# Kernel optimization log

Hardware: AMD Instinct MI355X
Metric: run time of the kernel (lower is better)

## Reference

```python
import jax, jax.numpy as jnp
import numpy as np

N = 100000    # total nodes
E = 1600000   # total edges
B = 64        # graphs in batch
F_IN = 64     # node feature dim (input_shape)
F_E = 16      # edge feature dim (edge_shape)
A = 6         # action dim (action_shape)
H = 16        # hidden_channels
L = 4         # num GEN layers
EPS = 1e-7    # GENConv message eps


def _ln(x, g, b):
    mu = x.mean(-1, keepdims=True)
    var = x.var(-1, keepdims=True)
    return (x - mu) * jax.lax.rsqrt(var + 1e-5) * g + b


def _genconv(x, src, dst, ea, t, w1, b1, g1, be1, w2, b2):
    # GENConv with softmax aggregation: msg = relu(x_j + e) + eps,
    # alpha = scatter_softmax(t*msg, dst), aggr = scatter_sum(msg*alpha),
    # out = MLP(x + aggr) with MLP = Lin(H,2H) -> LN -> ReLU -> Lin(2H,H)
    msg = jax.nn.relu(x[src] + ea) + EPS                      # [E,H]
    z = t * msg
    m = jax.ops.segment_max(z, dst, num_segments=N)           # [N,H]
    e = jnp.exp(z - m[dst])
    s = jax.ops.segment_sum(e, dst, num_segments=N)
    alpha = e / (s[dst] + 1e-16)
    aggr = jax.ops.segment_sum(msg * alpha, dst, num_segments=N)
    h = x + aggr
    h = jax.nn.relu(_ln(h @ w1 + b1, g1, be1))
    return h @ w2 + b2


def setup_inputs() -> dict:
    key = jax.random.key(0)
    ks = jax.random.split(key, 20)
    def rn(k, shape, scale=0.1):
        return jax.random.normal(k, shape, dtype=jnp.float32) * scale
    return {
        "x": rn(ks[0], (N, F_IN), 1.0),
        "edge_attr": rn(ks[1], (E, F_E), 1.0),
        "edge_index": jax.random.randint(ks[2], (2, E), 0, N),
        "batch": (jnp.arange(N) * B) // N,  # sorted, every graph non-empty
        "action": rn(ks[3], (B, A), 1.0),
        "node_w": rn(ks[4], (F_IN, H)), "node_b": rn(ks[5], (H,)),
        "edge_w": rn(ks[6], (F_E, H)), "edge_b": rn(ks[7], (H,)),
        "t": jnp.ones((L,), jnp.float32),
        "mlp_w1": rn(ks[8], (L, H, 2 * H)), "mlp_b1": rn(ks[9], (L, 2 * H)),
        "mlp_g1": jnp.ones((L, 2 * H), jnp.float32),
        "mlp_be1": jnp.zeros((L, 2 * H), jnp.float32),
        "mlp_w2": rn(ks[10], (L, 2 * H, H)), "mlp_b2": rn(ks[11], (L, H)),
        "ln_g": jnp.ones((L, H), jnp.float32), "ln_b": jnp.zeros((L, H), jnp.float32),
        "pin_w": rn(ks[12], (2 * H, 128)), "pin_b": rn(ks[13], (128,)),
        "ph_w": rn(ks[14], (128 + A, 10)), "ph_b": rn(ks[15], (10,)),
        "po_w": rn(ks[16], (10, 1)), "po_b": rn(ks[17], (1,)),
    }


def reference(x, edge_attr, edge_index, batch, action, node_w, node_b, edge_w,
              edge_b, t, mlp_w1, mlp_b1, mlp_g1, mlp_be1, mlp_w2, mlp_b2,
              ln_g, ln_b, pin_w, pin_b, ph_w, ph_b, po_w, po_b):
    src, dst = edge_index[0], edge_index[1]
    h = x @ node_w + node_b
    ea = edge_attr @ edge_w + edge_b
    # layer 0: bare conv (as in original forward)
    h = _genconv(h, src, dst, ea, t[0], mlp_w1[0], mlp_b1[0], mlp_g1[0],
                 mlp_be1[0], mlp_w2[0], mlp_b2[0])
    # layers 1..3: DeepGCN 'res+' blocks: x + conv(relu(norm(x)))
    for i in range(1, L):
        y = jax.nn.relu(_ln(h, ln_g[i], ln_b[i]))
        h = h + _genconv(y, src, dst, ea, t[i], mlp_w1[i], mlp_b1[i],
                         mlp_g1[i], mlp_be1[i], mlp_w2[i], mlp_b2[i])
    # final norm + act from layer 0 (dropout disabled: eval mode)
    h = jax.nn.relu(_ln(h, ln_g[0], ln_b[0]))
    # global max + mean pooling per graph
    gmp = jax.ops.segment_max(h, batch, num_segments=B)
    cnt = jax.ops.segment_sum(jnp.ones((N, 1), h.dtype), batch, num_segments=B)
    gap = jax.ops.segment_sum(h, batch, num_segments=B) / cnt
    mol = jnp.concatenate([gmp, gap], axis=1)                 # [B, 32]
    fp = jax.nn.relu(mol @ pin_w + pin_b)                     # [B, 128]
    pol = jax.nn.relu(jnp.concatenate([fp, action], axis=1) @ ph_w + ph_b)
    return pol @ po_w + po_b                                  # [B, 1]
```

## Files before the change

### kernel.cpp

```cpp
#include <hip/hip_runtime.h>
#include <hip/hip_fp16.h>

#define N_NODES 100000
#define N_EDGES 1600000
#define NB 64
#define F_INn 64
#define HID 16
#define NL 4
#define NSCAN_BLK 391
#define NBIN 256
#define BINW 391
#define NPBLK 256

__device__ __forceinline__ unsigned pack2h(float a, float b) {
    __half2 h = __floats2half2_rn(a, b);
    return *reinterpret_cast<unsigned*>(&h);
}

__device__ __forceinline__ void blk_range(int blk, int& e0, int& e1) {
    e0 = (int)(((long long)blk * N_EDGES) / NPBLK);
    e1 = (int)(((long long)(blk + 1) * N_EDGES) / NPBLK);
}

__global__ __launch_bounds__(256) void k_embed(
    const float* __restrict__ x, const float* __restrict__ nw,
    const float* __restrict__ nb, float* __restrict__ yout)
{
    __shared__ float xs[16 * 64];
    __shared__ float Wn[64 * 16];
    __shared__ float Bn[16];
    const int tid = threadIdx.x;
    for (int i = tid; i < 1024; i += 256) Wn[i] = nw[i];
    if (tid < 16) Bn[tid] = nb[tid];
    const int n0 = blockIdx.x * 16;
    reinterpret_cast<float4*>(xs)[tid] =
        reinterpret_cast<const float4*>(x + (size_t)n0 * F_INn)[tid];
    __syncthreads();
    const int nl = tid >> 4, j = tid & 15;
    float acc = Bn[j];
    #pragma unroll 8
    for (int k = 0; k < 64; ++k) acc += xs[nl * 64 + k] * Wn[k * 16 + j];
    yout[(size_t)(n0 + nl) * HID + j] = acc;
}

__global__ __launch_bounds__(256) void k_hist1(
    const int* __restrict__ dstA, int* __restrict__ histG)
{
    __shared__ int h[NBIN];
    const int tid = threadIdx.x, blk = blockIdx.x;
    for (int t = tid; t < NBIN; t += 256) h[t] = 0;
    __syncthreads();
    int e0, e1; blk_range(blk, e0, e1);
    for (int e = e0 + tid; e < e1; e += 256)
        atomicAdd(&h[dstA[e] / BINW], 1);
    __syncthreads();
    for (int t = tid; t < NBIN; t += 256) histG[blk * NBIN + t] = h[t];
}

__global__ __launch_bounds__(NPBLK) void k_scanblk(
    const int* __restrict__ histG, int* __restrict__ boffsG,
    int* __restrict__ binTot)
{
    __shared__ int sc[NPBLK];
    const int tid = threadIdx.x, bin = blockIdx.x;
    const int v = histG[tid * NBIN + bin];
    sc[tid] = v;
    __syncthreads();
    for (int off = 1; off < NPBLK; off <<= 1) {
        int t = (tid >= off) ? sc[tid - off] : 0;
        __syncthreads();
        sc[tid] += t;
        __syncthreads();
    }
    boffsG[tid * NBIN + bin] = sc[tid] - v;
    if (tid == NPBLK - 1) binTot[bin] = sc[tid];
}

__global__ __launch_bounds__(NBIN) void k_scanbin(
    const int* __restrict__ binTot, int* __restrict__ binStart)
{
    __shared__ int sc[NBIN];
    const int tid = threadIdx.x;
    const int v = binTot[tid];
    sc[tid] = v;
    __syncthreads();
    for (int off = 1; off < NBIN; off <<= 1) {
        int t = (tid >= off) ? sc[tid - off] : 0;
        __syncthreads();
        sc[tid] += t;
        __syncthreads();
    }
    binStart[tid] = sc[tid] - v;
    if (tid == NBIN - 1) binStart[NBIN] = sc[tid];
}

__global__ __launch_bounds__(256) void k_partl(
    const int* __restrict__ dstA, const int* __restrict__ srcA,
    const int* __restrict__ boffsG, const int* __restrict__ binStart,
    int2* __restrict__ partK)
{
    __shared__ int cur[NBIN];
    const int tid = threadIdx.x, blk = blockIdx.x;
    for (int t = tid; t < NBIN; t += 256)
        cur[t] = binStart[t] + boffsG[blk * NBIN + t];
    __syncthreads();
    int e0, e1; blk_range(blk, e0, e1);
    for (int e = e0 + tid; e < e1; e += 256) {
        const int d = dstA[e];
        const int bin = d / BINW;
        const int dloc = d - bin * BINW;
        const int p = atomicAdd(&cur[bin], 1);
        partK[p] = make_int2(srcA[e], (dloc << 21) | e);
    }
}

__global__ __launch_bounds__(512) void k_finishl(
    const int2* __restrict__ partK, const int* __restrict__ binStart,
    int* __restrict__ rowptr, int* __restrict__ srcP, int* __restrict__ csrE)
{
    __shared__ int h[BINW];
    __shared__ int sc[512];
    __shared__ int cur[BINW];
    const int tid = threadIdx.x, bin = blockIdx.x;
    const int base = bin * BINW;
    for (int t = tid; t < BINW; t += 512) h[t] = 0;
    __syncthreads();
    const int i0 = binStart[bin], i1 = binStart[bin + 1];
    for (int i = i0 + tid; i < i1; i += 512)
        atomicAdd(&h[partK[i].y >> 21], 1);
    __syncthreads();
    const int v = (tid < BINW) ? h[tid] : 0;
    sc[tid] = v;
    __syncthreads();
    for (int off = 1; off < 512; off <<= 1) {
        int t = (tid >= off) ? sc[tid - off] : 0;
        __syncthreads();
        sc[tid] += t;
        __syncthreads();
    }
    if (tid < BINW) {
        const int r = i0 + sc[tid] - v;
        const int idx = base + tid;
        if (idx < N_NODES) rowptr[idx] = r;
        cur[tid] = r;
    }
    if (bin == NBIN - 1 && tid == 0) rowptr[N_NODES] = N_EDGES;
    __syncthreads();
    for (int i = i0 + tid; i < i1; i += 512) {
        const int2 w = partK[i];
        const int dloc = w.y >> 21;
        const int p = atomicAdd(&cur[dloc], 1);
        srcP[p] = w.x;
        csrE[p] = w.y & 0x1FFFFF;
    }
}

__global__ __launch_bounds__(256) void k_permea(
    const int* __restrict__ csrE, const float* __restrict__ eattr,
    const float* __restrict__ ew, const float* __restrict__ ebv,
    __half* __restrict__ eaPh)
{
    __shared__ float EW[256];
    __shared__ float EB[16];
    const int tid = threadIdx.x;
    EW[tid] = ew[tid];
    if (tid < 16) EB[tid] = ebv[tid];
    __syncthreads();
    const int p = blockIdx.x * 256 + tid;
    const int e = csrE[p];
    float acc[16];
    #pragma unroll
    for (int j = 0; j < 16; ++j) acc[j] = EB[j];
    const float4* ag = reinterpret_cast<const float4*>(eattr + ((size_t)e << 4));
    #pragma unroll
    for (int q = 0; q < 4; ++q) {
        const float4 av = ag[q];
        #pragma unroll
        for (int j = 0; j < 16; ++j) {
            acc[j] += av.x * EW[(q * 4 + 0) * 16 + j];
            acc[j] += av.y * EW[(q * 4 + 1) * 16 + j];
            acc[j] += av.z * EW[(q * 4 + 2) * 16 + j];
            acc[j] += av.w * EW[(q * 4 + 3) * 16 + j];
        }
    }
    uint4 lo, hi;
    lo.x = pack2h(acc[0], acc[1]);   lo.y = pack2h(acc[2], acc[3]);
    lo.z = pack2h(acc[4], acc[5]);   lo.w = pack2h(acc[6], acc[7]);
    hi.x = pack2h(acc[8], acc[9]);   hi.y = pack2h(acc[10], acc[11]);
    hi.z = pack2h(acc[12], acc[13]); hi.w = pack2h(acc[14], acc[15]);
    uint4* eo = reinterpret_cast<uint4*>(eaPh) + ((size_t)p << 1);
    eo[0] = lo;
    eo[1] = hi;
}

__global__ __launch_bounds__(256) void k_count(
    const int* __restrict__ dstA, int* __restrict__ cnt)
{
    const int e = blockIdx.x * 256 + threadIdx.x;
    if (e < N_EDGES) atomicAdd(cnt + dstA[e], 1);
}

__global__ __launch_bounds__(256) void k_scan1(
    const int* __restrict__ cnt, int* __restrict__ rowptr, int* __restrict__ bsum)
{
    __shared__ int sc[256];
    const int tid = threadIdx.x;
    const int i = blockIdx.x * 256 + tid;
    const int v = (i < N_NODES) ? cnt[i] : 0;
    sc[tid] = v;
    __syncthreads();
    for (int off = 1; off < 256; off <<= 1) {
        int t = (tid >= off) ? sc[tid - off] : 0;
        __syncthreads();
        sc[tid] += t;
        __syncthreads();
    }
    if (i < N_NODES) rowptr[i] = sc[tid] - v;
    if (tid == 255) bsum[blockIdx.x] = sc[tid];
}

__global__ __launch_bounds__(512) void k_scan2(
    const int* __restrict__ bsum, int* __restrict__ offs, int* __restrict__ rowptr)
{
    __shared__ int sc[512];
    const int tid = threadIdx.x;
    const int v = (tid < NSCAN_BLK) ? bsum[tid] : 0;
    sc[tid] = v;
    __syncthreads();
    for (int off = 1; off < 512; off <<= 1) {
        int t = (tid >= off) ? sc[tid - off] : 0;
        __syncthreads();
        sc[tid] += t;
        __syncthreads();
    }
    if (tid < NSCAN_BLK) offs[tid] = sc[tid] - v;
    if (tid == NSCAN_BLK - 1) rowptr[N_NODES] = sc[tid];
}

__global__ __launch_bounds__(256) void k_scan3(
    int* __restrict__ rowptr, const int* __restrict__ offs, int* __restrict__ cnt)
{
    const int i = blockIdx.x * 256 + threadIdx.x;
    if (i < N_NODES) {
        rowptr[i] += offs[i >> 8];
        cnt[i] = 0;
    }
}

__global__ __launch_bounds__(256) void k_fill(
    const int* __restrict__ dstA, const int* __restrict__ rowptr,
    int* __restrict__ cnt, int* __restrict__ csr)
{
    const int e = blockIdx.x * 256 + threadIdx.x;
    if (e >= N_EDGES) return;
    const int d = dstA[e];
    const int pos = atomicAdd(cnt + d, 1);
    csr[rowptr[d] + pos] = e;
}

__global__ __launch_bounds__(256, 8) void k_aggr(
    const float* __restrict__ yin, const int* __restrict__ rowptr,
    const int* __restrict__ srcP, const __half* __restrict__ eaPh,
    const float* __restrict__ tArr, int layer, float* __restrict__ aggr)
{
    const int t = blockIdx.x * 256 + threadIdx.x;
    const int n = t >> 4;
    if (n >= N_NODES) return;
    const int sub = threadIdx.x & 15;
    const int es = sub >> 2, cg = sub & 3;
    const int row0 = rowptr[n], row1 = rowptr[n + 1];
    const float tv = tArr[layer];

    float4 s = make_float4(0.f, 0.f, 0.f, 0.f);
    float4 num = make_float4(0.f, 0.f, 0.f, 0.f);

    int i = row0 + es;
    bool has = (i < row1);
    int spn = 0;
    uint2 ean = make_uint2(0u, 0u);
    if (has) {
        spn = srcP[i];
        ean = reinterpret_cast<const uint2*>(eaPh + ((size_t)i << 4))[cg];
    }
    while (has) {
        const int sp = spn;
        const uint2 eaw = ean;
        const int i2 = i + 4;
        const bool has2 = (i2 < row1);
        if (has2) {
            spn = srcP[i2];
            ean = reinterpret_cast<const uint2*>(eaPh + ((size_t)i2 << 4))[cg];
        }
        const float4 yv = reinterpret_cast<const float4*>(yin + ((size_t)sp << 4))[cg];
        const float2 f0 = __half22float2(*reinterpret_cast<const __half2*>(&eaw.x));
        const float2 f1 = __half22float2(*reinterpret_cast<const __half2*>(&eaw.y));
        float m, ez;
        m = fmaxf(yv.x + f0.x, 0.f) + 1e-7f; ez = __expf(tv * m); s.x += ez; num.x += m * ez;
        m = fmaxf(yv.y + f0.y, 0.f) + 1e-7f; ez = __expf(tv * m); s.y += ez; num.y += m * ez;
        m = fmaxf(yv.z + f1.x, 0.f) + 1e-7f; ez = __expf(tv * m); s.z += ez; num.z += m * ez;
        m = fmaxf(yv.w + f1.y, 0.f) + 1e-7f; ez = __expf(tv * m); s.w += ez; num.w += m * ez;
        i = i2; has = has2;
    }
    s.x += __shfl_xor(s.x, 4); s.y += __shfl_xor(s.y, 4);
    s.z += __shfl_xor(s.z, 4); s.w += __shfl_xor(s.w, 4);
    num.x += __shfl_xor(num.x, 4); num.y += __shfl_xor(num.y, 4);
    num.z += __shfl_xor(num.z, 4); num.w += __shfl_xor(num.w, 4);
    s.x += __shfl_xor(s.x, 8); s.y += __shfl_xor(s.y, 8);
    s.z += __shfl_xor(s.z, 8); s.w += __shfl_xor(s.w, 8);
    num.x += __shfl_xor(num.x, 8); num.y += __shfl_xor(num.y, 8);
    num.z += __shfl_xor(num.z, 8); num.w += __shfl_xor(num.w, 8);
    if (es == 0) {
        float4 r;
        r.x = num.x / (s.x + 1e-16f);
        r.y = num.y / (s.y + 1e-16f);
        r.z = num.z / (s.z + 1e-16f);
        r.w = num.w / (s.w + 1e-16f);
        reinterpret_cast<float4*>(aggr + ((size_t)n << 4))[cg] = r;
    }
}

__global__ __launch_bounds__(256) void k_node(
    const float* __restrict__ yin, const float* __restrict__ hprev,
    const float* __restrict__ aggr,
    const float* __restrict__ w1, const float* __restrict__ b1,
    const float* __restrict__ g1, const float* __restrict__ be1,
    const float* __restrict__ w2, const float* __restrict__ b2,
    const float* __restrict__ gn, const float* __restrict__ bn,
    float* __restrict__ hout, float* __restrict__ yout, int layer)
{
    __shared__ float4 W1[128];
    __shared__ float4 W2[128];
    __shared__ float B1[32], G1[32], BE1[32], B2[16], GN[16], BN[16];
    const int tid = threadIdx.x;
    if (tid < 128) {
        W1[tid] = reinterpret_cast<const float4*>(w1)[tid];
        W2[tid] = reinterpret_cast<const float4*>(w2)[tid];
    }
    if (tid < 32) { B1[tid] = b1[tid]; G1[tid] = g1[tid]; BE1[tid] = be1[tid]; }
    if (tid < 16) { B2[tid] = b2[tid]; GN[tid] = gn[tid]; BN[tid] = bn[tid]; }
    __syncthreads();
    const int n = blockIdx.x * 256 + tid;
    if (n >= N_NODES) return;
    const size_t base = (size_t)n * HID;

    float hin[16];
    {
        const float4* yg = reinterpret_cast<const float4*>(yin + base);
        const float4* ag = reinterpret_cast<const float4*>(aggr + base);
        #pragma unroll
        for (int q = 0; q < 4; ++q) {
            float4 yv = yg[q], av = ag[q];
            hin[q * 4 + 0] = yv.x + av.x;
            hin[q * 4 + 1] = yv.y + av.y;
            hin[q * 4 + 2] = yv.z + av.z;
            hin[q * 4 + 3] = yv.w + av.w;
        }
    }
    float z[32];
    #pragma unroll
    for (int i = 0; i < 32; ++i) z[i] = B1[i];
    #pragma unroll
    for (int j = 0; j < 16; ++j) {
        const float hv = hin[j];
        #pragma unroll
        for (int q = 0; q < 8; ++q) {
            float4 w = W1[j * 8 + q];
            z[q * 4 + 0] += hv * w.x; z[q * 4 + 1] += hv * w.y;
            z[q * 4 + 2] += hv * w.z; z[q * 4 + 3] += hv * w.w;
        }
    }
    float mu = 0.f;
    #pragma unroll
    for (int i = 0; i < 32; ++i) mu += z[i];
    mu *= (1.f / 32.f);
    float var = 0.f;
    #pragma unroll
    for (int i = 0; i < 32; ++i) { float d = z[i] - mu; var += d * d; }
    var *= (1.f / 32.f);
    const float rs = rsqrtf(var + 1e-5f);

    float o[16];
    #pragma unroll
    for (int j = 0; j < 16; ++j) o[j] = B2[j];
    #pragma unroll
    for (int i = 0; i < 32; ++i) {
        const float r = fmaxf((z[i] - mu) * rs * G1[i] + BE1[i], 0.f);
        #pragma unroll
        for (int q = 0; q < 4; ++q) {
            float4 w = W2[i * 4 + q];
            o[q * 4 + 0] += r * w.x; o[q * 4 + 1] += r * w.y;
            o[q * 4 + 2] += r * w.z; o[q * 4 + 3] += r * w.w;
        }
    }
    float hn[16];
    if (layer == 0) {
        #pragma unroll
        for (int j = 0; j < 16; ++j) hn[j] = o[j];
    } else {
        const float4* hg = reinterpret_cast<const float4*>(hprev + base);
        float hr[16];
        *reinterpret_cast<float4*>(&hr[0])  = hg[0];
        *reinterpret_cast<float4*>(&hr[4])  = hg[1];
        *reinterpret_cast<float4*>(&hr[8])  = hg[2];
        *reinterpret_cast<float4*>(&hr[12]) = hg[3];
        #pragma unroll
        for (int j = 0; j < 16; ++j) hn[j] = hr[j] + o[j];
    }
    {
        float4* ho = reinterpret_cast<float4*>(hout + base);
        #pragma unroll
        for (int q = 0; q < 4; ++q)
            ho[q] = make_float4(hn[q*4+0], hn[q*4+1], hn[q*4+2], hn[q*4+3]);
    }
    float mu2 = 0.f;
    #pragma unroll
    for (int j = 0; j < 16; ++j) mu2 += hn[j];
    mu2 *= (1.f / 16.f);
    float v2 = 0.f;
    #pragma unroll
    for (int j = 0; j < 16; ++j) { float d = hn[j] - mu2; v2 += d * d; }
    v2 *= (1.f / 16.f);
    const float rs2 = rsqrtf(v2 + 1e-5f);
    float yn[16];
    #pragma unroll
    for (int j = 0; j < 16; ++j)
        yn[j] = fmaxf((hn[j] - mu2) * rs2 * GN[j] + BN[j], 0.f);
    {
        float4* yo = reinterpret_cast<float4*>(yout + base);
        #pragma unroll
        for (int q = 0; q < 4; ++q)
            yo[q] = make_float4(yn[q*4+0], yn[q*4+1], yn[q*4+2], yn[q*4+3]);
    }
}

__global__ __launch_bounds__(256) void k_layer(
    const float* __restrict__ yin, const float* __restrict__ hprev,
    const int* __restrict__ rowptr, const int* __restrict__ csr,
    const int* __restrict__ srcA, const float* __restrict__ eattr,
    const float* __restrict__ ew, const float* __restrict__ ebv,
    const float* __restrict__ tArr, int layer,
    const float* __restrict__ w1, const float* __restrict__ b1,
    const float* __restrict__ g1, const float* __restrict__ be1,
    const float* __restrict__ w2, const float* __restrict__ b2,
    const float* __restrict__ gn, const float* __restrict__ bn,
    float* __restrict__ hout, float* __restrict__ yout)
{
    __shared__ float EW[256];
    __shared__ float EB[16];
    __shared__ float4 W1[128];
    __shared__ float4 W2[128];
    __shared__ float B1[32], G1[32], BE1[32], B2[16], GN[16], BN[16];
    const int tid = threadIdx.x;
    EW[tid] = ew[tid];
    if (tid < 128) {
        W1[tid] = reinterpret_cast<const float4*>(w1)[tid];
        W2[tid] = reinterpret_cast<const float4*>(w2)[tid];
    }
    if (tid < 32) { B1[tid] = b1[tid]; G1[tid] = g1[tid]; BE1[tid] = be1[tid]; }
    if (tid < 16) { EB[tid] = ebv[tid]; B2[tid] = b2[tid]; GN[tid] = gn[tid]; BN[tid] = bn[tid]; }
    __syncthreads();

    const int t = blockIdx.x * 256 + tid;
    const int n = t >> 2, sub = t & 3;
    if (n >= N_NODES) return;
    const int row0 = rowptr[n], row1 = rowptr[n + 1];
    const float tv = tArr[layer];

    float s[16], num[16];
    #pragma unroll
    for (int j = 0; j < 16; ++j) { s[j] = 0.f; num[j] = 0.f; }

    for (int i = row0 + sub; i < row1; i += 4) {
        const int eid = csr[i];
        const int sp = srcA[eid];
        float a[16], yv[16];
        {
            const float4* ag = reinterpret_cast<const float4*>(eattr + (size_t)eid * 16);
            *reinterpret_cast<float4*>(&a[0])  = ag[0];
            *reinterpret_cast<float4*>(&a[4])  = ag[1];
            *reinterpret_cast<float4*>(&a[8])  = ag[2];
            *reinterpret_cast<float4*>(&a[12]) = ag[3];
            const float4* yg = reinterpret_cast<const float4*>(yin + (size_t)sp * 16);
            *reinterpret_cast<float4*>(&yv[0])  = yg[0];
            *reinterpret_cast<float4*>(&yv[4])  = yg[1];
            *reinterpret_cast<float4*>(&yv[8])  = yg[2];
            *reinterpret_cast<float4*>(&yv[12]) = yg[3];
        }
        float acc[16];
        #pragma unroll
        for (int j = 0; j < 16; ++j) acc[j] = EB[j];
        #pragma unroll
        for (int k = 0; k < 16; ++k) {
            const float av = a[k];
            #pragma unroll
            for (int j = 0; j < 16; ++j) acc[j] += av * EW[k * 16 + j];
        }
        #pragma unroll
        for (int j = 0; j < 16; ++j) {
            float m = fmaxf(yv[j] + acc[j], 0.f) + 1e-7f;
            float ez = __expf(tv * m);
            s[j] += ez;
            num[j] += m * ez;
        }
    }
    #pragma unroll
    for (int j = 0; j < 16; ++j) {
        s[j]   += __shfl_xor(s[j], 1);   num[j] += __shfl_xor(num[j], 1);
        s[j]   += __shfl_xor(s[j], 2);   num[j] += __shfl_xor(num[j], 2);
    }
    if (sub != 0) return;

    const size_t base = (size_t)n * HID;
    float hin[16];
    {
        const float4* yg = reinterpret_cast<const float4*>(yin + base);
        float yr[16];
        *reinterpret_cast<float4*>(&yr[0])  = yg[0];
        *reinterpret_cast<float4*>(&yr[4])  = yg[1];
        *reinterpret_cast<float4*>(&yr[8])  = yg[2];
        *reinterpret_cast<float4*>(&yr[12]) = yg[3];
        #pragma unroll
        for (int j = 0; j < 16; ++j) hin[j] = yr[j] + num[j] / (s[j] + 1e-16f);
    }
    float z[32];
    #pragma unroll
    for (int i = 0; i < 32; ++i) z[i] = B1[i];
    #pragma unroll
    for (int j = 0; j < 16; ++j) {
        const float hv = hin[j];
        #pragma unroll
        for (int q = 0; q < 8; ++q) {
            float4 w = W1[j * 8 + q];
            z[q * 4 + 0] += hv * w.x; z[q * 4 + 1] += hv * w.y;
            z[q * 4 + 2] += hv * w.z; z[q * 4 + 3] += hv * w.w;
        }
    }
    float mu = 0.f;
    #pragma unroll
    for (int i = 0; i < 32; ++i) mu += z[i];
    mu *= (1.f / 32.f);
    float var = 0.f;
    #pragma unroll
    for (int i = 0; i < 32; ++i) { float d = z[i] - mu; var += d * d; }
    var *= (1.f / 32.f);
    const float rs = rsqrtf(var + 1e-5f);

    float o[16];
    #pragma unroll
    for (int j = 0; j < 16; ++j) o[j] = B2[j];
    #pragma unroll
    for (int i = 0; i < 32; ++i) {
        const float r = fmaxf((z[i] - mu) * rs * G1[i] + BE1[i], 0.f);
        #pragma unroll
        for (int q = 0; q < 4; ++q) {
            float4 w = W2[i * 4 + q];
            o[q * 4 + 0] += r * w.x; o[q * 4 + 1] += r * w.y;
            o[q * 4 + 2] += r * w.z; o[q * 4 + 3] += r * w.w;
        }
    }
    float hn[16];
    if (layer == 0) {
        #pragma unroll
        for (int j = 0; j < 16; ++j) hn[j] = o[j];
    } else {
        const float4* hg = reinterpret_cast<const float4*>(hprev + base);
        float hr[16];
        *reinterpret_cast<float4*>(&hr[0])  = hg[0];
        *reinterpret_cast<float4*>(&hr[4])  = hg[1];
        *reinterpret_cast<float4*>(&hr[8])  = hg[2];
        *reinterpret_cast<float4*>(&hr[12]) = hg[3];
        #pragma unroll
        for (int j = 0; j < 16; ++j) hn[j] = hr[j] + o[j];
    }
    {
        float4* ho = reinterpret_cast<float4*>(hout + base);
        #pragma unroll
        for (int q = 0; q < 4; ++q)
            ho[q] = make_float4(hn[q*4+0], hn[q*4+1], hn[q*4+2], hn[q*4+3]);
    }
    float mu2 = 0.f;
    #pragma unroll
    for (int j = 0; j < 16; ++j) mu2 += hn[j];
    mu2 *= (1.f / 16.f);
    float v2 = 0.f;
    #pragma unroll
    for (int j = 0; j < 16; ++j) { float d = hn[j] - mu2; v2 += d * d; }
    v2 *= (1.f / 16.f);
    const float rs2 = rsqrtf(v2 + 1e-5f);
    float yn[16];
    #pragma unroll
    for (int j = 0; j < 16; ++j)
        yn[j] = fmaxf((hn[j] - mu2) * rs2 * GN[j] + BN[j], 0.f);
    {
        float4* yo = reinterpret_cast<float4*>(yout + base);
        #pragma unroll
        for (int q = 0; q < 4; ++q)
            yo[q] = make_float4(yn[q*4+0], yn[q*4+1], yn[q*4+2], yn[q*4+3]);
    }
}

__global__ __launch_bounds__(256) void k_pool(
    const float* __restrict__ y, const int* __restrict__ batch,
    float* __restrict__ gmax, float* __restrict__ gsum, float* __restrict__ gcnt)
{
    const int g = blockIdx.x;
    const int tid = threadIdx.x;
    int lo = 0, hi = N_NODES;
    while (lo < hi) { int mid = (lo + hi) >> 1; if (batch[mid] < g) lo = mid + 1; else hi = mid; }
    const int start = lo;
    lo = 0; hi = N_NODES;
    while (lo < hi) { int mid = (lo + hi) >> 1; if (batch[mid] < g + 1) lo = mid + 1; else hi = mid; }
    const int end = lo;

    const int ch = tid & 15, slot = tid >> 4;
    float mx = 0.f, sm = 0.f;
    for (int n = start + slot; n < end; n += 16) {
        float v = y[(size_t)n * HID + ch];
        mx = fmaxf(mx, v);
        sm += v;
    }
    __shared__ float rm[256], rsum[256];
    rm[tid] = mx; rsum[tid] = sm;
    __syncthreads();
    for (int off = 8; off >= 1; off >>= 1) {
        if (slot < off) {
            rm[tid] = fmaxf(rm[tid], rm[tid + off * 16]);
            rsum[tid] += rsum[tid + off * 16];
        }
        __syncthreads();
    }
    if (slot == 0) {
        gmax[g * HID + ch] = rm[ch];
        gsum[g * HID + ch] = rsum[ch];
        if (ch == 0) gcnt[g] = (float)(end - start);
    }
}

__global__ __launch_bounds__(128) void k_final(
    const float* __restrict__ gmax, const float* __restrict__ gsum,
    const float* __restrict__ gcnt, const float* __restrict__ action,
    const float* __restrict__ pin_w, const float* __restrict__ pin_b,
    const float* __restrict__ ph_w, const float* __restrict__ ph_b,
    const float* __restrict__ po_w, const float* __restrict__ po_b,
    float* __restrict__ out)
{
    __shared__ float mol[32];
    __shared__ float fpv[128];
    __shared__ float pol[10];
    const int b = blockIdx.x, tid = threadIdx.x;
    if (tid < 16) mol[tid] = gmax[b * 16 + tid];
    else if (tid < 32) mol[tid] = gsum[b * 16 + (tid - 16)] / gcnt[b];
    __syncthreads();
    float acc = pin_b[tid];
    #pragma unroll 4
    for (int k = 0; k < 32; ++k) acc += mol[k] * pin_w[k * 128 + tid];
    fpv[tid] = fmaxf(acc, 0.f);
    __syncthreads();
    if (tid < 10) {
        float a2 = ph_b[tid];
        for (int k = 0; k < 128; ++k) a2 += fpv[k] * ph_w[k * 10 + tid];
        #pragma unroll
        for (int k = 0; k < 6; ++k) a2 += action[b * 6 + k] * ph_w[(128 + k) * 10 + tid];
        pol[tid] = fmaxf(a2, 0.f);
    }
    __syncthreads();
    if (tid == 0) {
        float o = po_b[0];
        #pragma unroll
        for (int i = 0; i < 10; ++i) o += pol[i] * po_w[i];
        out[b] = o;
    }
}

extern "C" void kernel_launch(void* const* d_in, const int* in_sizes, int n_in,
                              void* d_out, int out_size, void* d_ws, size_t ws_size,
                              hipStream_t stream)
{
    const float* x       = (const float*)d_in[0];
    const float* eattr   = (const float*)d_in[1];
    const int*   eidx    = (const int*)d_in[2];
    const int*   batch   = (const int*)d_in[3];
    const float* action  = (const float*)d_in[4];
    const float* node_w  = (const float*)d_in[5];
    const float* node_b  = (const float*)d_in[6];
    const float* edge_w  = (const float*)d_in[7];
    const float* edge_b  = (const float*)d_in[8];
    const float* tArr    = (const float*)d_in[9];
    const float* mlp_w1  = (const float*)d_in[10];
    const float* mlp_b1  = (const float*)d_in[11];
    const float* mlp_g1  = (const float*)d_in[12];
    const float* mlp_be1 = (const float*)d_in[13];
    const float* mlp_w2  = (const float*)d_in[14];
    const float* mlp_b2  = (const float*)d_in[15];
    const float* ln_g    = (const float*)d_in[16];
    const float* ln_b    = (const float*)d_in[17];
    const float* pin_w   = (const float*)d_in[18];
    const float* pin_b   = (const float*)d_in[19];
    const float* ph_w    = (const float*)d_in[20];
    const float* ph_b    = (const float*)d_in[21];
    const float* po_w    = (const float*)d_in[22];
    const float* po_b    = (const float*)d_in[23];
    float* out = (float*)d_out;

    char* ws = (char*)d_ws;
    float* h      = (float*)ws;
    float* y      = h + (size_t)N_NODES * HID;
    float* aggr   = y + (size_t)N_NODES * HID;
    int*   cnt    = (int*)(aggr + (size_t)N_NODES * HID);
    int*   rowptr = cnt + N_NODES;
    int*   bsum   = rowptr + N_NODES + 1;
    int*   offs   = bsum + NSCAN_BLK;
    int*   csr    = offs + NSCAN_BLK + 1;
    float* gmax   = (float*)(csr + N_EDGES);
    float* gsum   = gmax + NB * HID;
    float* gcnt   = gsum + NB * HID;
    int*   srcP   = (int*)(gcnt + NB);
    int*   csrE   = srcP + N_EDGES;
    __half* eaPh  = (__half*)(csrE + N_EDGES);
    const size_t need = (size_t)((char*)(eaPh + (size_t)N_EDGES * HID) - ws);
    const bool fast = (ws_size >= need);
    (void)in_sizes; (void)n_in; (void)out_size;

    int2* partK   = (int2*)h;
    int* histG    = (int*)aggr;
    int* boffsG   = histG + NPBLK * NBIN;
    int* binTot   = csr;
    int* binStart = csr + NBIN;

    const int* srcA = eidx;
    const int* dstA = eidx + N_EDGES;

    if (fast) {
        k_hist1<<<NPBLK, 256, 0, stream>>>(dstA, histG);
        k_scanblk<<<NBIN, NPBLK, 0, stream>>>(histG, boffsG, binTot);
        k_scanbin<<<1, NBIN, 0, stream>>>(binTot, binStart);
        k_partl<<<NPBLK, 256, 0, stream>>>(dstA, srcA, boffsG, binStart, partK);
        k_finishl<<<NBIN, 512, 0, stream>>>(partK, binStart, rowptr, srcP, csrE);
        k_permea<<<N_EDGES / 256, 256, 0, stream>>>(csrE, eattr, edge_w,
            edge_b, eaPh);
        k_embed<<<N_NODES / 16, 256, 0, stream>>>(x, node_w, node_b, y);
        const int gridA = (16 * N_NODES + 255) / 256;
        const int gridN = (N_NODES + 255) / 256;
        for (int l = 0; l < NL; ++l) {
            const int nidx = (l < 3) ? (l + 1) : 0;
            k_aggr<<<gridA, 256, 0, stream>>>(y, rowptr, srcP, eaPh, tArr, l, aggr);
            k_node<<<gridN, 256, 0, stream>>>(y, h, aggr,
                mlp_w1 + l * 512, mlp_b1 + l * 32, mlp_g1 + l * 32, mlp_be1 + l * 32,
                mlp_w2 + l * 512, mlp_b2 + l * 16, ln_g + nidx * 16, ln_b + nidx * 16,
                h, y, l);
        }
        k_pool<<<NB, 256, 0, stream>>>(y, batch, gmax, gsum, gcnt);
    } else {
        hipMemsetAsync(cnt, 0, (size_t)N_NODES * sizeof(int), stream);
        k_count<<<(N_EDGES + 255) / 256, 256, 0, stream>>>(dstA, cnt);
        k_scan1<<<NSCAN_BLK, 256, 0, stream>>>(cnt, rowptr, bsum);
        k_scan2<<<1, 512, 0, stream>>>(bsum, offs, rowptr);
        k_scan3<<<NSCAN_BLK, 256, 0, stream>>>(rowptr, offs, cnt);
        k_fill<<<(N_EDGES + 255) / 256, 256, 0, stream>>>(dstA, rowptr, cnt, csr);
        float* yA = y;
        float* yB = aggr;
        k_embed<<<N_NODES / 16, 256, 0, stream>>>(x, node_w, node_b, yA);
        const int grid = (4 * N_NODES + 255) / 256;
        for (int l = 0; l < NL; ++l) {
            const float* yin = (l & 1) ? yB : yA;
            float* yout      = (l & 1) ? yA : yB;
            const int nidx = (l < 3) ? (l + 1) : 0;
            k_layer<<<grid, 256, 0, stream>>>(
                yin, h, rowptr, csr, srcA, eattr, edge_w, edge_b, tArr, l,
                mlp_w1 + l * 512, mlp_b1 + l * 32, mlp_g1 + l * 32, mlp_be1 + l * 32,
                mlp_w2 + l * 512, mlp_b2 + l * 16, ln_g + nidx * 16, ln_b + nidx * 16,
                h, yout);
        }
        k_pool<<<NB, 256, 0, stream>>>(yA, batch, gmax, gsum, gcnt);
    }
    k_final<<<NB, 128, 0, stream>>>(gmax, gsum, gcnt, action,
        pin_w, pin_b, ph_w, ph_b, po_w, po_b, out);
}
```

Baseline: 347.5 us.

## Fuse edge aggregation and node MLP into one kernel with ping-pong y buffers

Merges k_aggr and k_node into k_laggr. After the shuffle reduction, the four lanes holding each node's aggregate run the node MLP and both layer norms cooperatively, exchanging values with wave shuffles. This drops the aggr buffer round-trip through global memory and one launch per layer. The y buffers now alternate between layers to avoid read/write races. The cost is that only a quarter of the lanes do the MLP, the 8-waves occupancy hint is gone, and every block now loads the weights into shared memory.

```diff
diff --git a/kernel.cpp b/kernel.cpp
--- a/kernel.cpp
+++ b/kernel.cpp
@@ -258,15 +258,30 @@
     csr[rowptr[d] + pos] = e;
 }
 
-__global__ __launch_bounds__(256, 8) void k_aggr(
-    const float* __restrict__ yin, const int* __restrict__ rowptr,
-    const int* __restrict__ srcP, const __half* __restrict__ eaPh,
-    const float* __restrict__ tArr, int layer, float* __restrict__ aggr)
-{
-    const int t = blockIdx.x * 256 + threadIdx.x;
+__global__ __launch_bounds__(256) void k_laggr(
+    const float* __restrict__ yin, float* __restrict__ hio,
+    const int* __restrict__ rowptr, const int* __restrict__ srcP,
+    const __half* __restrict__ eaPh, const float* __restrict__ tArr, int layer,
+    const float* __restrict__ w1, const float* __restrict__ b1,
+    const float* __restrict__ g1, const float* __restrict__ be1,
+    const float* __restrict__ w2, const float* __restrict__ b2,
+    const float* __restrict__ gn, const float* __restrict__ bn,
+    float* __restrict__ yout)
+{
+    __shared__ float W1s[512];
+    __shared__ float W2s[512];
+    __shared__ float B1[32], G1[32], BE1[32], B2[16], GN[16], BN[16];
+    const int tid = threadIdx.x;
+    W1s[tid] = w1[tid]; W1s[tid + 256] = w1[tid + 256];
+    W2s[tid] = w2[tid]; W2s[tid + 256] = w2[tid + 256];
+    if (tid < 32) { B1[tid] = b1[tid]; G1[tid] = g1[tid]; BE1[tid] = be1[tid]; }
+    if (tid < 16) { B2[tid] = b2[tid]; GN[tid] = gn[tid]; BN[tid] = bn[tid]; }
+    __syncthreads();
+
+    const int t = blockIdx.x * 256 + tid;
     const int n = t >> 4;
     if (n >= N_NODES) return;
-    const int sub = threadIdx.x & 15;
+    const int sub = tid & 15;
     const int es = sub >> 2, cg = sub & 3;
     const int row0 = rowptr[n], row1 = rowptr[n + 1];
     const float tv = tArr[layer];
@@ -309,128 +324,80 @@
     s.z += __shfl_xor(s.z, 8); s.w += __shfl_xor(s.w, 8);
     num.x += __shfl_xor(num.x, 8); num.y += __shfl_xor(num.y, 8);
     num.z += __shfl_xor(num.z, 8); num.w += __shfl_xor(num.w, 8);
-    if (es == 0) {
-        float4 r;
-        r.x = num.x / (s.x + 1e-16f);
-        r.y = num.y / (s.y + 1e-16f);
-        r.z = num.z / (s.z + 1e-16f);
-        r.w = num.w / (s.w + 1e-16f);
-        reinterpret_cast<float4*>(aggr + ((size_t)n << 4))[cg] = r;
-    }
-}
-
-__global__ __launch_bounds__(256) void k_node(
-    const float* __restrict__ yin, const float* __restrict__ hprev,
-    const float* __restrict__ aggr,
-    const float* __restrict__ w1, const float* __restrict__ b1,
-    const float* __restrict__ g1, const float* __restrict__ be1,
-    const float* __restrict__ w2, const float* __restrict__ b2,
-    const float* __restrict__ gn, const float* __restrict__ bn,
-    float* __restrict__ hout, float* __restrict__ yout, int layer)
-{
-    __shared__ float4 W1[128];
-    __shared__ float4 W2[128];
-    __shared__ float B1[32], G1[32], BE1[32], B2[16], GN[16], BN[16];
-    const int tid = threadIdx.x;
-    if (tid < 128) {
-        W1[tid] = reinterpret_cast<const float4*>(w1)[tid];
-        W2[tid] = reinterpret_cast<const float4*>(w2)[tid];
-    }
-    if (tid < 32) { B1[tid] = b1[tid]; G1[tid] = g1[tid]; BE1[tid] = be1[tid]; }
-    if (tid < 16) { B2[tid] = b2[tid]; GN[tid] = gn[tid]; BN[tid] = bn[tid]; }
-    __syncthreads();
-    const int n = blockIdx.x * 256 + tid;
-    if (n >= N_NODES) return;
+    if (es != 0) return;
+
+    const int lane = tid & 63;
+    const int g16 = lane & 48;
     const size_t base = (size_t)n * HID;
-
-    float hin[16];
+    float hin4[4];
     {
-        const float4* yg = reinterpret_cast<const float4*>(yin + base);
-        const float4* ag = reinterpret_cast<const float4*>(aggr + base);
-        #pragma unroll
-        for (int q = 0; q < 4; ++q) {
-            float4 yv = yg[q], av = ag[q];
-            hin[q * 4 + 0] = yv.x + av.x;
-            hin[q * 4 + 1] = yv.y + av.y;
-            hin[q * 4 + 2] = yv.z + av.z;
-            hin[q * 4 + 3] = yv.w + av.w;
-        }
-    }
-    float z[32];
-    #pragma unroll
-    for (int i = 0; i < 32; ++i) z[i] = B1[i];
+        const float4 yv = reinterpret_cast<const float4*>(yin + base)[cg];
+        hin4[0] = yv.x + num.x / (s.x + 1e-16f);
+        hin4[1] = yv.y + num.y / (s.y + 1e-16f);
+        hin4[2] = yv.z + num.z / (s.z + 1e-16f);
+        hin4[3] = yv.w + num.w / (s.w + 1e-16f);
+    }
+    float z8[8];
+    #pragma unroll
+    for (int c = 0; c < 8; ++c) z8[c] = B1[cg * 8 + c];
     #pragma unroll
     for (int j = 0; j < 16; ++j) {
-        const float hv = hin[j];
-        #pragma unroll
-        for (int q = 0; q < 8; ++q) {
-            float4 w = W1[j * 8 + q];
-            z[q * 4 + 0] += hv * w.x; z[q * 4 + 1] += hv * w.y;
-            z[q * 4 + 2] += hv * w.z; z[q * 4 + 3] += hv * w.w;
-        }
-    }
-    float mu = 0.f;
-    #pragma unroll
-    for (int i = 0; i < 32; ++i) mu += z[i];
-    mu *= (1.f / 32.f);
-    float var = 0.f;
-    #pragma unroll
-    for (int i = 0; i < 32; ++i) { float d = z[i] - mu; var += d * d; }
-    var *= (1.f / 32.f);
-    const float rs = rsqrtf(var + 1e-5f);
-
-    float o[16];
-    #pragma unroll
-    for (int j = 0; j < 16; ++j) o[j] = B2[j];
-    #pragma unroll
-    for (int i = 0; i < 32; ++i) {
-        const float r = fmaxf((z[i] - mu) * rs * G1[i] + BE1[i], 0.f);
-        #pragma unroll
-        for (int q = 0; q < 4; ++q) {
-            float4 w = W2[i * 4 + q];
-            o[q * 4 + 0] += r * w.x; o[q * 4 + 1] += r * w.y;
-            o[q * 4 + 2] += r * w.z; o[q * 4 + 3] += r * w.w;
-        }
-    }
-    float hn[16];
+        const float hv = __shfl(hin4[j & 3], g16 + (j >> 2), 64);
+        const float* wrow = &W1s[j * 32 + cg * 8];
+        #pragma unroll
+        for (int c = 0; c < 8; ++c) z8[c] += hv * wrow[c];
+    }
+    float ps = 0.f;
+    #pragma unroll
+    for (int c = 0; c < 8; ++c) ps += z8[c];
+    ps += __shfl_xor(ps, 1); ps += __shfl_xor(ps, 2);
+    const float mu = ps * (1.f / 32.f);
+    float pv = 0.f;
+    #pragma unroll
+    for (int c = 0; c < 8; ++c) { float d = z8[c] - mu; pv += d * d; }
+    pv += __shfl_xor(pv, 1); pv += __shfl_xor(pv, 2);
+    const float rs = rsqrtf(pv * (1.f / 32.f) + 1e-5f);
+
+    float r8[8];
+    #pragma unroll
+    for (int c = 0; c < 8; ++c)
+        r8[c] = fmaxf((z8[c] - mu) * rs * G1[cg * 8 + c] + BE1[cg * 8 + c], 0.f);
+
+    float o4[4];
+    #pragma unroll
+    for (int k = 0; k < 4; ++k) o4[k] = B2[cg * 4 + k];
+    #pragma unroll
+    for (int i2 = 0; i2 < 32; ++i2) {
+        const float rv = __shfl(r8[i2 & 7], g16 + (i2 >> 3), 64);
+        const float* wrow = &W2s[i2 * 16 + cg * 4];
+        #pragma unroll
+        for (int k = 0; k < 4; ++k) o4[k] += rv * wrow[k];
+    }
+    float hn4[4];
     if (layer == 0) {
         #pragma unroll
-        for (int j = 0; j < 16; ++j) hn[j] = o[j];
+        for (int k = 0; k < 4; ++k) hn4[k] = o4[k];
     } else {
-        const float4* hg = reinterpret_cast<const float4*>(hprev + base);
-        float hr[16];
-        *reinterpret_cast<float4*>(&hr[0])  = hg[0];
-        *reinterpret_cast<float4*>(&hr[4])  = hg[1];
-        *reinterpret_cast<float4*>(&hr[8])  = hg[2];
-        *reinterpret_cast<float4*>(&hr[12]) = hg[3];
-        #pragma unroll
-        for (int j = 0; j < 16; ++j) hn[j] = hr[j] + o[j];
-    }
-    {
-        float4* ho = reinterpret_cast<float4*>(hout + base);
-        #pragma unroll
-        for (int q = 0; q < 4; ++q)
-            ho[q] = make_float4(hn[q*4+0], hn[q*4+1], hn[q*4+2], hn[q*4+3]);
-    }
-    float mu2 = 0.f;
-    #pragma unroll
-    for (int j = 0; j < 16; ++j) mu2 += hn[j];
-    mu2 *= (1.f / 16.f);
-    float v2 = 0.f;
-    #pragma unroll
-    for (int j = 0; j < 16; ++j) { float d = hn[j] - mu2; v2 += d * d; }
-    v2 *= (1.f / 16.f);
-    const float rs2 = rsqrtf(v2 + 1e-5f);
-    float yn[16];
-    #pragma unroll
-    for (int j = 0; j < 16; ++j)
-        yn[j] = fmaxf((hn[j] - mu2) * rs2 * GN[j] + BN[j], 0.f);
-    {
-        float4* yo = reinterpret_cast<float4*>(yout + base);
-        #pragma unroll
-        for (int q = 0; q < 4; ++q)
-            yo[q] = make_float4(yn[q*4+0], yn[q*4+1], yn[q*4+2], yn[q*4+3]);
-    }
+        const float4 hv = reinterpret_cast<const float4*>(hio + base)[cg];
+        hn4[0] = hv.x + o4[0]; hn4[1] = hv.y + o4[1];
+        hn4[2] = hv.z + o4[2]; hn4[3] = hv.w + o4[3];
+    }
+    reinterpret_cast<float4*>(hio + base)[cg] =
+        make_float4(hn4[0], hn4[1], hn4[2], hn4[3]);
+    float ps2 = hn4[0] + hn4[1] + hn4[2] + hn4[3];
+    ps2 += __shfl_xor(ps2, 1); ps2 += __shfl_xor(ps2, 2);
+    const float mu2 = ps2 * (1.f / 16.f);
+    float pv2 = 0.f;
+    #pragma unroll
+    for (int k = 0; k < 4; ++k) { float d = hn4[k] - mu2; pv2 += d * d; }
+    pv2 += __shfl_xor(pv2, 1); pv2 += __shfl_xor(pv2, 2);
+    const float rs2 = rsqrtf(pv2 * (1.f / 16.f) + 1e-5f);
+    float yn4[4];
+    #pragma unroll
+    for (int k = 0; k < 4; ++k)
+        yn4[k] = fmaxf((hn4[k] - mu2) * rs2 * GN[cg * 4 + k] + BN[cg * 4 + k], 0.f);
+    reinterpret_cast<float4*>(yout + base)[cg] =
+        make_float4(yn4[0], yn4[1], yn4[2], yn4[3]);
 }
 
 __global__ __launch_bounds__(256) void k_layer(
@@ -704,9 +671,9 @@
 
     char* ws = (char*)d_ws;
     float* h      = (float*)ws;
-    float* y      = h + (size_t)N_NODES * HID;
-    float* aggr   = y + (size_t)N_NODES * HID;
-    int*   cnt    = (int*)(aggr + (size_t)N_NODES * HID);
+    float* yA     = h + (size_t)N_NODES * HID;
+    float* yB     = yA + (size_t)N_NODES * HID;
+    int*   cnt    = (int*)(yB + (size_t)N_NODES * HID);
     int*   rowptr = cnt + N_NODES;
     int*   bsum   = rowptr + N_NODES + 1;
     int*   offs   = bsum + NSCAN_BLK;
@@ -722,7 +689,7 @@
     (void)in_sizes; (void)n_in; (void)out_size;
 
     int2* partK   = (int2*)h;
-    int* histG    = (int*)aggr;
+    int* histG    = (int*)yB;
     int* boffsG   = histG + NPBLK * NBIN;
     int* binTot   = csr;
     int* binStart = csr + NBIN;
@@ -738,18 +705,19 @@
         k_finishl<<<NBIN, 512, 0, stream>>>(partK, binStart, rowptr, srcP, csrE);
         k_permea<<<N_EDGES / 256, 256, 0, stream>>>(csrE, eattr, edge_w,
             edge_b, eaPh);
-        k_embed<<<N_NODES / 16, 256, 0, stream>>>(x, node_w, node_b, y);
+        k_embed<<<N_NODES / 16, 256, 0, stream>>>(x, node_w, node_b, yA);
         const int gridA = (16 * N_NODES + 255) / 256;
-        const int gridN = (N_NODES + 255) / 256;
         for (int l = 0; l < NL; ++l) {
+            const float* yin = (l & 1) ? yB : yA;
+            float* yout      = (l & 1) ? yA : yB;
             const int nidx = (l < 3) ? (l + 1) : 0;
-            k_aggr<<<gridA, 256, 0, stream>>>(y, rowptr, srcP, eaPh, tArr, l, aggr);
-            k_node<<<gridN, 256, 0, stream>>>(y, h, aggr,
+            k_laggr<<<gridA, 256, 0, stream>>>(yin, h, rowptr, srcP, eaPh,
+                tArr, l,
                 mlp_w1 + l * 512, mlp_b1 + l * 32, mlp_g1 + l * 32, mlp_be1 + l * 32,
                 mlp_w2 + l * 512, mlp_b2 + l * 16, ln_g + nidx * 16, ln_b + nidx * 16,
-                h, y, l);
-        }
-        k_pool<<<NB, 256, 0, stream>>>(y, batch, gmax, gsum, gcnt);
+                yout);
+        }
+        k_pool<<<NB, 256, 0, stream>>>(yA, batch, gmax, gsum, gcnt);
     } else {
         hipMemsetAsync(cnt, 0, (size_t)N_NODES * sizeof(int), stream);
         k_count<<<(N_EDGES + 255) / 256, 256, 0, stream>>>(dstA, cnt);
@@ -757,8 +725,6 @@
         k_scan2<<<1, 512, 0, stream>>>(bsum, offs, rowptr);
         k_scan3<<<NSCAN_BLK, 256, 0, stream>>>(rowptr, offs, cnt);
         k_fill<<<(N_EDGES + 255) / 256, 256, 0, stream>>>(dstA, rowptr, cnt, csr);
-        float* yA = y;
-        float* yB = aggr;
         k_embed<<<N_NODES / 16, 256, 0, stream>>>(x, node_w, node_b, yA);
         const int grid = (4 * N_NODES + 255) / 256;
         for (int l = 0; l < NL; ++l) {
```

Measured after the change: 350.4 us. Within noise of the previous version (+0.8%).
